# Kernel tuning notes

Hardware: AMD Instinct MI355X
Metric: run time of the kernel (lower is better)

Reference implementation:

```python
import jax, jax.numpy as jnp
import numpy as np

N_NODES = 100000
N_EDGES = 3200000
IN_DIM, HID_DIM, LAT_DIM = 128, 64, 64


def gcn_conv(x, edge_index, W, b):
    """PyG-style GCNConv: add self-loops, symmetric deg^-1/2 normalization,
    linear transform, scatter-add aggregation, bias."""
    N = x.shape[0]
    loops = jnp.arange(N, dtype=edge_index.dtype)
    src = jnp.concatenate([edge_index[0], loops])  # [E+N]
    dst = jnp.concatenate([edge_index[1], loops])  # [E+N]
    # degree on target index (with self loops)
    deg = jax.ops.segment_sum(jnp.ones_like(dst, dtype=x.dtype), dst, num_segments=N)
    dinv = jnp.where(deg > 0, jax.lax.rsqrt(deg), 0.0)
    norm = dinv[src] * dinv[dst]  # [E+N]
    h = x @ W  # [N, out_dim] -- transform BEFORE gather (out_dim <= in_dim)
    msg = h[src] * norm[:, None]  # [E+N, out_dim]
    out = jax.ops.segment_sum(msg, dst, num_segments=N)
    return out + b


def setup_inputs() -> dict:
    key = jax.random.key(0)
    ks = jax.random.split(key, 6)
    x = jax.random.normal(ks[0], (N_NODES, IN_DIM), dtype=jnp.float32)
    edge_index = jax.random.randint(ks[1], (2, N_EDGES), 0, N_NODES, dtype=jnp.int64)
    # Glorot-ish init for weights, zero bias (PyG default)
    W1 = jax.random.normal(ks[2], (IN_DIM, HID_DIM), dtype=jnp.float32) / np.sqrt(IN_DIM)
    b1 = jnp.zeros((HID_DIM,), dtype=jnp.float32)
    W2 = jax.random.normal(ks[3], (HID_DIM, LAT_DIM), dtype=jnp.float32) / np.sqrt(HID_DIM)
    b2 = jnp.zeros((LAT_DIM,), dtype=jnp.float32)
    return {"x": x, "edge_index": edge_index, "W1": W1, "b1": b1, "W2": W2, "b2": b2}


def reference(x, edge_index, W1, b1, W2, b2):
    h = jax.nn.relu(gcn_conv(x, edge_index, W1, b1))
    return gcn_conv(h, edge_index, W2, b2)
```

## Files before the change

### kernel.cpp

```cpp
#include <hip/hip_runtime.h>
#include <cstdint>


#define BSHIFT 7
#define NBMAX 784
#define CH 4096
#define MAXB 6016

typedef __attribute__((ext_vector_type(8))) short bf16x8;
typedef __attribute__((ext_vector_type(4))) float f32x4;

__device__ inline unsigned short f2bf(float f) {
    unsigned u = __float_as_uint(f);
    unsigned r = (u + 0x7FFFu + ((u >> 16) & 1u)) >> 16;
    return (unsigned short)r;
}
__device__ inline unsigned pack2(float a, float b) {
    return (unsigned)f2bf(a) | ((unsigned)f2bf(b) << 16);
}
__device__ inline float blo(unsigned u) { return __uint_as_float(u << 16); }
__device__ inline float bhi(unsigned u) { return __uint_as_float(u & 0xFFFF0000u); }

__global__ __launch_bounds__(256) void hist_kernel(const int* __restrict__ dst,
                                                   int* __restrict__ histmat,
                                                   int E, int nb, int nblk,
                                                   const float* __restrict__ W1,
                                                   const float* __restrict__ W2,
                                                   unsigned short* __restrict__ W1t,
                                                   unsigned short* __restrict__ W2t) {
    if (blockIdx.x >= (unsigned)nblk) {
        int i = (blockIdx.x - nblk) * 256 + threadIdx.x;
        if (i < 128 * 64) {
            int k = i >> 6, n = i & 63;
            W1t[n * 128 + k] = f2bf(W1[i]);
        }
        int j = i - 128 * 64;
        if (j >= 0 && j < 64 * 64) {
            int k = j >> 6, n = j & 63;
            W2t[n * 64 + k] = f2bf(W2[j]);
        }
        return;
    }
    __shared__ int hist[NBMAX];
    int t = threadIdx.x;
    for (int b = t; b < nb; b += 256) hist[b] = 0;
    __syncthreads();
    int base = blockIdx.x * CH;
#pragma unroll
    for (int j = 0; j < CH / 1024; ++j) {
        int idx = base + j * 1024 + t * 4;
        if (idx + 4 <= E) {
            int4 d = *(const int4*)(dst + idx);
            atomicAdd(&hist[d.x >> BSHIFT], 1);
            atomicAdd(&hist[d.y >> BSHIFT], 1);
            atomicAdd(&hist[d.z >> BSHIFT], 1);
            atomicAdd(&hist[d.w >> BSHIFT], 1);
        } else {
            for (int k = 0; k < 4; ++k)
                if (idx + k < E) atomicAdd(&hist[dst[idx + k] >> BSHIFT], 1);
        }
    }
    __syncthreads();
    for (int b = t; b < nb; b += 256) histmat[blockIdx.x * nb + b] = hist[b];
}

__global__ __launch_bounds__(256) void scancol_kernel(const int* __restrict__ histmat,
                                                      int* __restrict__ colbase,
                                                      int* __restrict__ buckettotal,
                                                      int nb, int nblk) {
    __shared__ int ts[256];
    int b = blockIdx.x;
    int t = threadIdx.x;
    int v[4];
    int tsum = 0;
#pragma unroll
    for (int k = 0; k < 4; ++k) {
        int blk = t * 4 + k;
        v[k] = (blk < nblk) ? histmat[blk * nb + b] : 0;
        tsum += v[k];
    }
    ts[t] = tsum;
    __syncthreads();
    for (int ofs = 1; ofs < 256; ofs <<= 1) {
        int val = (t >= ofs) ? ts[t - ofs] : 0;
        __syncthreads();
        ts[t] += val;
        __syncthreads();
    }
    int run = ts[t] - tsum;
#pragma unroll
    for (int k = 0; k < 4; ++k) {
        int blk = t * 4 + k;
        if (blk < nblk) colbase[blk * nb + b] = run;
        run += v[k];
    }
    if (t == 255) buckettotal[b] = ts[255];
}

__global__ __launch_bounds__(256) void scanbucket_kernel(const int* __restrict__ buckettotal,
                                                         int* __restrict__ bucketbase,
                                                         int nb, int E) {
    __shared__ int ts[256];
    int t = threadIdx.x;
    int v[4];
    int tsum = 0;
#pragma unroll
    for (int k = 0; k < 4; ++k) {
        int b = t * 4 + k;
        v[k] = (b < nb) ? buckettotal[b] : 0;
        tsum += v[k];
    }
    ts[t] = tsum;
    __syncthreads();
    for (int ofs = 1; ofs < 256; ofs <<= 1) {
        int val = (t >= ofs) ? ts[t - ofs] : 0;
        __syncthreads();
        ts[t] += val;
        __syncthreads();
    }
    int run = ts[t] - tsum;
#pragma unroll
    for (int k = 0; k < 4; ++k) {
        int b = t * 4 + k;
        if (b < nb) bucketbase[b] = run;
        run += v[k];
    }
    if (t == 0) bucketbase[nb] = E;
}

__global__ __launch_bounds__(256) void bscatter_kernel(const int* __restrict__ src,
                                                       const int* __restrict__ dst,
                                                       const int* __restrict__ colbase,
                                                       const int* __restrict__ bucketbase,
                                                       int* __restrict__ packed,
                                                       int E, int nb) {
    __shared__ int cur[NBMAX];
    int t = threadIdx.x;
    for (int b = t; b < nb; b += 256)
        cur[b] = bucketbase[b] + colbase[blockIdx.x * nb + b];
    __syncthreads();
    int base = blockIdx.x * CH;
#pragma unroll
    for (int j = 0; j < CH / 1024; ++j) {
        int idx = base + j * 1024 + t * 4;
        if (idx + 4 <= E) {
            int4 d = *(const int4*)(dst + idx);
            int4 s = *(const int4*)(src + idx);
            int p;
            p = atomicAdd(&cur[d.x >> BSHIFT], 1); packed[p] = ((d.x & 127) << 17) | s.x;
            p = atomicAdd(&cur[d.y >> BSHIFT], 1); packed[p] = ((d.y & 127) << 17) | s.y;
            p = atomicAdd(&cur[d.z >> BSHIFT], 1); packed[p] = ((d.z & 127) << 17) | s.z;
            p = atomicAdd(&cur[d.w >> BSHIFT], 1); packed[p] = ((d.w & 127) << 17) | s.w;
        } else {
            for (int k = 0; k < 4; ++k)
                if (idx + k < E) {
                    int dd = dst[idx + k], ss = src[idx + k];
                    int p = atomicAdd(&cur[dd >> BSHIFT], 1);
                    packed[p] = ((dd & 127) << 17) | ss;
                }
        }
    }
}

__global__ __launch_bounds__(256) void bcsr_kernel(const int* __restrict__ packed,
                                                   const int* __restrict__ bucketbase,
                                                   int* __restrict__ rowptr,
                                                   float* __restrict__ dinv,
                                                   int* __restrict__ csr,
                                                   int N, int nb) {
    __shared__ int deg[128];
    __shared__ int lrp[128];
    __shared__ int ts[128];
    __shared__ int ebuf[MAXB];
    __shared__ int obuf[MAXB];
    int b = blockIdx.x;
    int t = threadIdx.x;
    if (t < 128) deg[t] = 0;
    __syncthreads();
    int bb0 = bucketbase[b];
    int bb1 = bucketbase[b + 1];
    int cnt = bb1 - bb0;
    bool fits = (cnt <= MAXB);
    if (fits) {
        for (int i = t; i < cnt; i += 256) {
            int v = packed[bb0 + i];
            ebuf[i] = v;
            atomicAdd(&deg[v >> 17], 1);
        }
    } else {
        for (int i = t; i < cnt; i += 256)
            atomicAdd(&deg[packed[bb0 + i] >> 17], 1);
    }
    __syncthreads();
    if (t < 128) ts[t] = deg[t];
    __syncthreads();
    for (int ofs = 1; ofs < 128; ofs <<= 1) {
        int v = (t < 128 && t >= ofs) ? ts[t - ofs] : 0;
        __syncthreads();
        if (t < 128) ts[t] += v;
        __syncthreads();
    }
    int node0 = b << BSHIFT;
    int nlocal = min(128, N - node0);
    if (t < 128) lrp[t] = ts[t] - deg[t];
    if (t < nlocal) {
        rowptr[node0 + t] = bb0 + (ts[t] - deg[t]);
        dinv[node0 + t] = rsqrtf((float)(deg[t] + 1));
    }
    if (t == nlocal) rowptr[node0 + nlocal] = bb1;
    __syncthreads();
    if (fits) {
        for (int i = t; i < cnt; i += 256) {
            int v = ebuf[i];
            int p = atomicAdd(&lrp[v >> 17], 1);
            obuf[p] = v & 0x1FFFF;
        }
        __syncthreads();
        for (int i = t; i < cnt; i += 256) csr[bb0 + i] = obuf[i];
    } else {
        for (int i = t; i < cnt; i += 256) {
            int v = packed[bb0 + i];
            int p = atomicAdd(&lrp[v >> 17], 1);
            csr[bb0 + p] = v & 0x1FFFF;
        }
    }
}

template <int K, bool XBF16>
__global__ __launch_bounds__(256) void gemm_mfma(const void* __restrict__ Xv,
                                                 const unsigned short* __restrict__ Wt,
                                                 const float* __restrict__ dinv,
                                                 unsigned short* __restrict__ Ybf, int M) {
    constexpr int KP = K + 8;
    __shared__ unsigned short Xs[64 * KP];
    __shared__ unsigned short Ws[64 * KP];
    int t = threadIdx.x;
    int row0 = blockIdx.x * 64;

    for (int i = t; i < 64 * K / 8; i += 256) {
        int r = i / (K / 8), c8 = i % (K / 8);
        *(uint4*)(&Ws[r * KP + c8 * 8]) = ((const uint4*)Wt)[i];
    }
    if (XBF16) {
        const unsigned short* X = (const unsigned short*)Xv;
        for (int i = t; i < 64 * K / 8; i += 256) {
            int r = i / (K / 8), c8 = i % (K / 8);
            int gr = row0 + r;
            uint4 v = make_uint4(0u, 0u, 0u, 0u);
            if (gr < M) v = ((const uint4*)(X + (size_t)gr * K))[c8];
            *(uint4*)(&Xs[r * KP + c8 * 8]) = v;
        }
    } else {
        const float* X = (const float*)Xv;
        for (int i = t; i < 64 * K / 4; i += 256) {
            int r = i / (K / 4), c4 = i % (K / 4);
            int gr = row0 + r;
            float4 v = make_float4(0.f, 0.f, 0.f, 0.f);
            if (gr < M) v = ((const float4*)(X + (size_t)gr * K))[c4];
            uint2 p;
            p.x = pack2(v.x, v.y);
            p.y = pack2(v.z, v.w);
            *(uint2*)(&Xs[r * KP + c4 * 4]) = p;
        }
    }
    __syncthreads();

    int lane = t & 63;
    int w = t >> 6;
    int m = lane & 15;
    int q = lane >> 4;

    f32x4 acc[4];
#pragma unroll
    for (int nt = 0; nt < 4; ++nt) acc[nt] = (f32x4){0.f, 0.f, 0.f, 0.f};

#pragma unroll
    for (int s = 0; s < K / 32; ++s) {
        bf16x8 a = *(const bf16x8*)(&Xs[(16 * w + m) * KP + s * 32 + q * 8]);
#pragma unroll
        for (int nt = 0; nt < 4; ++nt) {
            bf16x8 b = *(const bf16x8*)(&Ws[(16 * nt + m) * KP + s * 32 + q * 8]);
            acc[nt] = __builtin_amdgcn_mfma_f32_16x16x32_bf16(a, b, acc[nt], 0, 0, 0);
        }
    }
    __syncthreads();

    unsigned short* Cs = Xs;
#pragma unroll
    for (int nt = 0; nt < 4; ++nt)
#pragma unroll
        for (int r = 0; r < 4; ++r) {
            int row = 16 * w + q * 4 + r;
            int gr = row0 + row;
            float d = (gr < M) ? dinv[gr] : 0.f;
            Cs[row * 72 + nt * 16 + m] = f2bf(acc[nt][r] * d);
        }
    __syncthreads();
    for (int i = t; i < 64 * 64 / 8; i += 256) {
        int r = i >> 3, c8 = i & 7;
        int gr = row0 + r;
        if (gr < M)
            *(uint4*)(Ybf + (size_t)gr * 64 + c8 * 8) = *(const uint4*)(&Cs[r * 72 + c8 * 8]);
    }
}

__global__ __launch_bounds__(256) void aggregate_kernel(const unsigned* __restrict__ hsu,
                                                        const int* __restrict__ rowptr,
                                                        const int* __restrict__ csr,
                                                        const float* __restrict__ dinv,
                                                        const float* __restrict__ bias,
                                                        void* __restrict__ outv, int N,
                                                        int do_relu, int obf) {
    int t = threadIdx.x;
    int node = blockIdx.x * 32 + (t >> 3);
    if (node >= N) return;
    int sub = t & 7;
    int gbase = t & 56;

    float acc[8];
    {
        uint4 v = *(const uint4*)(hsu + (size_t)node * 32 + sub * 4);
        acc[0] = blo(v.x); acc[1] = bhi(v.x);
        acc[2] = blo(v.y); acc[3] = bhi(v.y);
        acc[4] = blo(v.z); acc[5] = bhi(v.z);
        acc[6] = blo(v.w); acc[7] = bhi(v.w);
    }
    int e0 = rowptr[node];
    int e1 = rowptr[node + 1];

    int e = e0;
    for (; e + 8 <= e1; e += 8) {
        int idx = csr[e + sub];
#pragma unroll
        for (int j = 0; j < 8; ++j) {
            int s = __shfl(idx, gbase + j, 64);
            uint4 v = *(const uint4*)(hsu + (size_t)s * 32 + sub * 4);
            acc[0] += blo(v.x); acc[1] += bhi(v.x);
            acc[2] += blo(v.y); acc[3] += bhi(v.y);
            acc[4] += blo(v.z); acc[5] += bhi(v.z);
            acc[6] += blo(v.w); acc[7] += bhi(v.w);
        }
    }
    for (; e < e1; ++e) {
        int s = csr[e];
        uint4 v = *(const uint4*)(hsu + (size_t)s * 32 + sub * 4);
        acc[0] += blo(v.x); acc[1] += bhi(v.x);
        acc[2] += blo(v.y); acc[3] += bhi(v.y);
        acc[4] += blo(v.z); acc[5] += bhi(v.z);
        acc[6] += blo(v.w); acc[7] += bhi(v.w);
    }

    float d = dinv[node];
    float4 b0 = *(const float4*)(bias + sub * 8);
    float4 b1 = *(const float4*)(bias + sub * 8 + 4);
    float o[8];
    o[0] = fmaf(acc[0], d, b0.x); o[1] = fmaf(acc[1], d, b0.y);
    o[2] = fmaf(acc[2], d, b0.z); o[3] = fmaf(acc[3], d, b0.w);
    o[4] = fmaf(acc[4], d, b1.x); o[5] = fmaf(acc[5], d, b1.y);
    o[6] = fmaf(acc[6], d, b1.z); o[7] = fmaf(acc[7], d, b1.w);
    if (do_relu) {
#pragma unroll
        for (int k = 0; k < 8; ++k) o[k] = fmaxf(o[k], 0.f);
    }
    if (obf) {
        unsigned short* outb = (unsigned short*)outv;
        uint4 p;
        p.x = pack2(o[0], o[1]); p.y = pack2(o[2], o[3]);
        p.z = pack2(o[4], o[5]); p.w = pack2(o[6], o[7]);
        *(uint4*)(outb + (size_t)node * 64 + sub * 8) = p;
    } else {
        float* op = (float*)outv + (size_t)node * 64 + sub * 8;
        *(float4*)(op)     = make_float4(o[0], o[1], o[2], o[3]);
        *(float4*)(op + 4) = make_float4(o[4], o[5], o[6], o[7]);
    }
}

extern "C" void kernel_launch(void* const* d_in, const int* in_sizes, int n_in,
                              void* d_out, int out_size, void* d_ws, size_t ws_size,
                              hipStream_t stream) {
    const float* x  = (const float*)d_in[0];
    const int*   ei = (const int*)d_in[1];
    const float* W1 = (const float*)d_in[2];
    const float* b1 = (const float*)d_in[3];
    const float* W2 = (const float*)d_in[4];
    const float* b2 = (const float*)d_in[5];

    const int N = in_sizes[0] / 128;
    const int E = in_sizes[1] / 2;
    const int* src = ei;
    const int* dst = ei + E;
    float* out = (float*)d_out;

    const int nb   = (N + 127) >> BSHIFT;
    const int nblk = (E + CH - 1) / CH;

    char* ws = (char*)d_ws;
    size_t off = 0;
    auto alloc = [&](size_t bytes) -> char* {
        char* p = ws + off;
        off = (off + bytes + 255) & ~(size_t)255;
        return p;
    };
    int*   csr         = (int*)alloc((size_t)E * 4);
    int*   rowptr      = (int*)alloc((size_t)(N + 1) * 4);
    float* dinv        = (float*)alloc((size_t)N * 4);
    int*   bucketbase  = (int*)alloc((size_t)(nb + 1) * 4);
    int*   buckettotal = (int*)alloc((size_t)nb * 4);
    unsigned short* W1t = (unsigned short*)alloc(64 * 128 * 2);
    unsigned short* W2t = (unsigned short*)alloc(64 * 64 * 2);
    unsigned short* bufA = (unsigned short*)alloc((size_t)N * 64 * 2);
    unsigned short* bufB = (unsigned short*)alloc((size_t)N * 64 * 2);
    int* histmat = (int*)bufA;
    int* packed  = (int*)((char*)bufA + ((size_t)nblk * nb * 4 + 255 & ~(size_t)255) + 256);

    hist_kernel<<<nblk + 48, 256, 0, stream>>>(dst, histmat, E, nb, nblk, W1, W2, W1t, W2t);
    scancol_kernel<<<nb, 256, 0, stream>>>(histmat, histmat, buckettotal, nb, nblk);
    scanbucket_kernel<<<1, 256, 0, stream>>>(buckettotal, bucketbase, nb, E);
    bscatter_kernel<<<nblk, 256, 0, stream>>>(src, dst, histmat, bucketbase, packed, E, nb);
    bcsr_kernel<<<nb, 256, 0, stream>>>(packed, bucketbase, rowptr, dinv, csr, N, nb);

    gemm_mfma<128, false><<<(N + 63) / 64, 256, 0, stream>>>(x, W1t, dinv, bufA, N);
    aggregate_kernel<<<(N + 31) / 32, 256, 0, stream>>>((const unsigned*)bufA, rowptr, csr,
                                                        dinv, b1, bufB, N, 1, 1);
    gemm_mfma<64, true><<<(N + 63) / 64, 256, 0, stream>>>(bufB, W2t, dinv, bufA, N);
    aggregate_kernel<<<(N + 31) / 32, 256, 0, stream>>>((const unsigned*)bufA, rowptr, csr,
                                                        dinv, b2, out, N, 0, 0);
}
```

Baseline: 318.8 us.

## Stage bucket scatter through shared memory and unroll gather loop by sixteen

The bucket scatter kernel now builds a local histogram per chunk, prefix-sums it, and groups the chunk's packed edges by bucket in shared memory. It then writes them out contiguously, so global stores become mostly coalesced runs instead of random per-edge stores. The aggregation kernel gains a 16-edge unrolled loop to keep more gather loads in flight. The cost is extra shared memory (about 40KB per block), which may lower occupancy, plus additional syncs and a second pass of LDS atomics.

```diff
diff --git a/kernel.cpp b/kernel.cpp
--- a/kernel.cpp
+++ b/kernel.cpp
@@ -134,32 +134,92 @@
                                                        const int* __restrict__ bucketbase,
                                                        int* __restrict__ packed,
                                                        int E, int nb) {
-    __shared__ int cur[NBMAX];
-    int t = threadIdx.x;
-    for (int b = t; b < nb; b += 256)
-        cur[b] = bucketbase[b] + colbase[blockIdx.x * nb + b];
-    __syncthreads();
+    __shared__ int lofs[NBMAX];
+    __shared__ int lcur[NBMAX];
+    __shared__ int vals[CH];
+    __shared__ int dlt[CH];
+    int t = threadIdx.x;
+    for (int b = t; b < nb; b += 256) lofs[b] = 0;
+    __syncthreads();
+
     int base = blockIdx.x * CH;
+    int n = min(CH, E - base);
+
+    int4 dreg[CH / 1024], sreg[CH / 1024];
 #pragma unroll
     for (int j = 0; j < CH / 1024; ++j) {
         int idx = base + j * 1024 + t * 4;
         if (idx + 4 <= E) {
-            int4 d = *(const int4*)(dst + idx);
-            int4 s = *(const int4*)(src + idx);
-            int p;
-            p = atomicAdd(&cur[d.x >> BSHIFT], 1); packed[p] = ((d.x & 127) << 17) | s.x;
-            p = atomicAdd(&cur[d.y >> BSHIFT], 1); packed[p] = ((d.y & 127) << 17) | s.y;
-            p = atomicAdd(&cur[d.z >> BSHIFT], 1); packed[p] = ((d.z & 127) << 17) | s.z;
-            p = atomicAdd(&cur[d.w >> BSHIFT], 1); packed[p] = ((d.w & 127) << 17) | s.w;
+            dreg[j] = *(const int4*)(dst + idx);
+            sreg[j] = *(const int4*)(src + idx);
+            atomicAdd(&lofs[dreg[j].x >> BSHIFT], 1);
+            atomicAdd(&lofs[dreg[j].y >> BSHIFT], 1);
+            atomicAdd(&lofs[dreg[j].z >> BSHIFT], 1);
+            atomicAdd(&lofs[dreg[j].w >> BSHIFT], 1);
         } else {
-            for (int k = 0; k < 4; ++k)
+            int* dp = (int*)&dreg[j];
+            int* sp = (int*)&sreg[j];
+            for (int k = 0; k < 4; ++k) {
+                dp[k] = -1;
                 if (idx + k < E) {
-                    int dd = dst[idx + k], ss = src[idx + k];
-                    int p = atomicAdd(&cur[dd >> BSHIFT], 1);
-                    packed[p] = ((dd & 127) << 17) | ss;
+                    dp[k] = dst[idx + k];
+                    sp[k] = src[idx + k];
+                    atomicAdd(&lofs[dp[k] >> BSHIFT], 1);
                 }
-        }
-    }
+            }
+        }
+    }
+    __syncthreads();
+
+    {
+        __shared__ int ts[256];
+        int v[4];
+        int tsum = 0;
+#pragma unroll
+        for (int k = 0; k < 4; ++k) {
+            int b = t * 4 + k;
+            v[k] = (b < nb) ? lofs[b] : 0;
+            tsum += v[k];
+        }
+        ts[t] = tsum;
+        __syncthreads();
+        for (int ofs = 1; ofs < 256; ofs <<= 1) {
+            int val = (t >= ofs) ? ts[t - ofs] : 0;
+            __syncthreads();
+            ts[t] += val;
+            __syncthreads();
+        }
+        int run = ts[t] - tsum;
+#pragma unroll
+        for (int k = 0; k < 4; ++k) {
+            int b = t * 4 + k;
+            if (b < nb) {
+                lcur[b] = run;
+                lofs[b] = bucketbase[b] + colbase[blockIdx.x * nb + b] - run;
+            }
+            run += v[k];
+        }
+    }
+    __syncthreads();
+
+#pragma unroll
+    for (int j = 0; j < CH / 1024; ++j) {
+        int* dp = (int*)&dreg[j];
+        int* sp = (int*)&sreg[j];
+#pragma unroll
+        for (int k = 0; k < 4; ++k) {
+            int dd = dp[k];
+            if (dd >= 0) {
+                int b = dd >> BSHIFT;
+                int slot = atomicAdd(&lcur[b], 1);
+                vals[slot] = ((dd & 127) << 17) | sp[k];
+                dlt[slot] = lofs[b];
+            }
+        }
+    }
+    __syncthreads();
+
+    for (int i = t; i < n; i += 256) packed[dlt[i] + i] = vals[i];
 }
 
 __global__ __launch_bounds__(256) void bcsr_kernel(const int* __restrict__ packed,
@@ -329,6 +389,19 @@
     int e1 = rowptr[node + 1];
 
     int e = e0;
+    for (; e + 16 <= e1; e += 16) {
+        int idxA = csr[e + sub];
+        int idxB = csr[e + 8 + sub];
+#pragma unroll
+        for (int j = 0; j < 16; ++j) {
+            int s = __shfl((j < 8) ? idxA : idxB, gbase + (j & 7), 64);
+            uint4 v = *(const uint4*)(hsu + (size_t)s * 32 + sub * 4);
+            acc[0] += blo(v.x); acc[1] += bhi(v.x);
+            acc[2] += blo(v.y); acc[3] += bhi(v.y);
+            acc[4] += blo(v.z); acc[5] += bhi(v.z);
+            acc[6] += blo(v.w); acc[7] += bhi(v.w);
+        }
+    }
     for (; e + 8 <= e1; e += 8) {
         int idx = csr[e + sub];
 #pragma unroll
```

Result: slower. 348.6 us (+9.4%).

## Replace per-block histogram matrix scan with global atomic bucket counts and local staging

Applied to the files above, without the earlier changes.

Replaces the per-block histogram matrix plus column scan with a grid-stride global histogram using atomics and a single bucket scan, folding the weight transpose into the scan kernel. The scatter kernel now computes its own local histogram, reserves global ranges per bucket via atomics, stages edges in shared memory grouped by bucket, then writes them out contiguously. This removes one kernel launch and the histmat read/write traffic, and turns scattered global writes into bucket-grouped runs. In exchange the edge order within each bucket is no longer deterministic, the scatter kernel needs about 70KB of shared memory (reducing occupancy), and the dst array is read twice in the scatter.

```diff
diff --git a/kernel.cpp b/kernel.cpp
--- a/kernel.cpp
+++ b/kernel.cpp
@@ -4,7 +4,7 @@
 
 #define BSHIFT 7
 #define NBMAX 784
-#define CH 4096
+#define CH 8192
 #define MAXB 6016
 
 typedef __attribute__((ext_vector_type(8))) short bf16x8;
@@ -21,34 +21,15 @@
 __device__ inline float blo(unsigned u) { return __uint_as_float(u << 16); }
 __device__ inline float bhi(unsigned u) { return __uint_as_float(u & 0xFFFF0000u); }
 
-__global__ __launch_bounds__(256) void hist_kernel(const int* __restrict__ dst,
-                                                   int* __restrict__ histmat,
-                                                   int E, int nb, int nblk,
-                                                   const float* __restrict__ W1,
-                                                   const float* __restrict__ W2,
-                                                   unsigned short* __restrict__ W1t,
-                                                   unsigned short* __restrict__ W2t) {
-    if (blockIdx.x >= (unsigned)nblk) {
-        int i = (blockIdx.x - nblk) * 256 + threadIdx.x;
-        if (i < 128 * 64) {
-            int k = i >> 6, n = i & 63;
-            W1t[n * 128 + k] = f2bf(W1[i]);
-        }
-        int j = i - 128 * 64;
-        if (j >= 0 && j < 64 * 64) {
-            int k = j >> 6, n = j & 63;
-            W2t[n * 64 + k] = f2bf(W2[j]);
-        }
-        return;
-    }
+__global__ __launch_bounds__(256) void ghist_kernel(const int* __restrict__ dst,
+                                                    int* __restrict__ bucketcount,
+                                                    int E, int nb) {
     __shared__ int hist[NBMAX];
     int t = threadIdx.x;
     for (int b = t; b < nb; b += 256) hist[b] = 0;
     __syncthreads();
-    int base = blockIdx.x * CH;
-#pragma unroll
-    for (int j = 0; j < CH / 1024; ++j) {
-        int idx = base + j * 1024 + t * 4;
+    int stride = gridDim.x * 1024;
+    for (int idx = blockIdx.x * 1024 + t * 4; idx < E; idx += stride) {
         if (idx + 4 <= E) {
             int4 d = *(const int4*)(dst + idx);
             atomicAdd(&hist[d.x >> BSHIFT], 1);
@@ -61,22 +42,41 @@
         }
     }
     __syncthreads();
-    for (int b = t; b < nb; b += 256) histmat[blockIdx.x * nb + b] = hist[b];
-}
-
-__global__ __launch_bounds__(256) void scancol_kernel(const int* __restrict__ histmat,
-                                                      int* __restrict__ colbase,
-                                                      int* __restrict__ buckettotal,
-                                                      int nb, int nblk) {
+    for (int b = t; b < nb; b += 256) {
+        int h = hist[b];
+        if (h) atomicAdd(&bucketcount[b], h);
+    }
+}
+
+__global__ __launch_bounds__(256) void scanbucket_kernel(const int* __restrict__ bucketcount,
+                                                         int* __restrict__ bucketbase,
+                                                         int* __restrict__ buckcur,
+                                                         int nb, int E,
+                                                         const float* __restrict__ W1,
+                                                         const float* __restrict__ W2,
+                                                         unsigned short* __restrict__ W1t,
+                                                         unsigned short* __restrict__ W2t) {
+    if (blockIdx.x > 0) {
+        int i = (blockIdx.x - 1) * 256 + threadIdx.x;
+        if (i < 128 * 64) {
+            int k = i >> 6, n = i & 63;
+            W1t[n * 128 + k] = f2bf(W1[i]);
+        }
+        int j = i - 128 * 64;
+        if (j >= 0 && j < 64 * 64) {
+            int k = j >> 6, n = j & 63;
+            W2t[n * 64 + k] = f2bf(W2[j]);
+        }
+        return;
+    }
     __shared__ int ts[256];
-    int b = blockIdx.x;
     int t = threadIdx.x;
     int v[4];
     int tsum = 0;
 #pragma unroll
     for (int k = 0; k < 4; ++k) {
-        int blk = t * 4 + k;
-        v[k] = (blk < nblk) ? histmat[blk * nb + b] : 0;
+        int b = t * 4 + k;
+        v[k] = (b < nb) ? bucketcount[b] : 0;
         tsum += v[k];
     }
     ts[t] = tsum;
@@ -90,39 +90,11 @@
     int run = ts[t] - tsum;
 #pragma unroll
     for (int k = 0; k < 4; ++k) {
-        int blk = t * 4 + k;
-        if (blk < nblk) colbase[blk * nb + b] = run;
-        run += v[k];
-    }
-    if (t == 255) buckettotal[b] = ts[255];
-}
-
-__global__ __launch_bounds__(256) void scanbucket_kernel(const int* __restrict__ buckettotal,
-                                                         int* __restrict__ bucketbase,
-                                                         int nb, int E) {
-    __shared__ int ts[256];
-    int t = threadIdx.x;
-    int v[4];
-    int tsum = 0;
-#pragma unroll
-    for (int k = 0; k < 4; ++k) {
         int b = t * 4 + k;
-        v[k] = (b < nb) ? buckettotal[b] : 0;
-        tsum += v[k];
-    }
-    ts[t] = tsum;
-    __syncthreads();
-    for (int ofs = 1; ofs < 256; ofs <<= 1) {
-        int val = (t >= ofs) ? ts[t - ofs] : 0;
-        __syncthreads();
-        ts[t] += val;
-        __syncthreads();
-    }
-    int run = ts[t] - tsum;
-#pragma unroll
-    for (int k = 0; k < 4; ++k) {
-        int b = t * 4 + k;
-        if (b < nb) bucketbase[b] = run;
+        if (b < nb) {
+            bucketbase[b] = run;
+            buckcur[b] = run;
+        }
         run += v[k];
     }
     if (t == 0) bucketbase[nb] = E;
@@ -130,36 +102,97 @@
 
 __global__ __launch_bounds__(256) void bscatter_kernel(const int* __restrict__ src,
                                                        const int* __restrict__ dst,
-                                                       const int* __restrict__ colbase,
-                                                       const int* __restrict__ bucketbase,
+                                                       int* __restrict__ buckcur,
                                                        int* __restrict__ packed,
                                                        int E, int nb) {
-    __shared__ int cur[NBMAX];
-    int t = threadIdx.x;
-    for (int b = t; b < nb; b += 256)
-        cur[b] = bucketbase[b] + colbase[blockIdx.x * nb + b];
-    __syncthreads();
+    __shared__ int lofs[NBMAX];
+    __shared__ int lcur[NBMAX];
+    __shared__ int vals[CH];
+    __shared__ int dlt[CH];
+    __shared__ int ts[256];
+    int t = threadIdx.x;
+    for (int b = t; b < nb; b += 256) lofs[b] = 0;
+    __syncthreads();
+
     int base = blockIdx.x * CH;
+    int n = min(CH, E - base);
+
+#pragma unroll
+    for (int j = 0; j < CH / 1024; ++j) {
+        int idx = base + j * 1024 + t * 4;
+        if (idx + 4 <= E) {
+            int4 d = *(const int4*)(dst + idx);
+            atomicAdd(&lofs[d.x >> BSHIFT], 1);
+            atomicAdd(&lofs[d.y >> BSHIFT], 1);
+            atomicAdd(&lofs[d.z >> BSHIFT], 1);
+            atomicAdd(&lofs[d.w >> BSHIFT], 1);
+        } else {
+            for (int k = 0; k < 4; ++k)
+                if (idx + k < E) atomicAdd(&lofs[dst[idx + k] >> BSHIFT], 1);
+        }
+    }
+    __syncthreads();
+
+    {
+        int v[4];
+        int tsum = 0;
+#pragma unroll
+        for (int k = 0; k < 4; ++k) {
+            int b = t * 4 + k;
+            v[k] = (b < nb) ? lofs[b] : 0;
+            tsum += v[k];
+        }
+        ts[t] = tsum;
+        __syncthreads();
+        for (int ofs = 1; ofs < 256; ofs <<= 1) {
+            int val = (t >= ofs) ? ts[t - ofs] : 0;
+            __syncthreads();
+            ts[t] += val;
+            __syncthreads();
+        }
+        int run = ts[t] - tsum;
+#pragma unroll
+        for (int k = 0; k < 4; ++k) {
+            int b = t * 4 + k;
+            if (b < nb) {
+                lcur[b] = run;
+                int g = v[k] ? atomicAdd(&buckcur[b], v[k]) : 0;
+                lofs[b] = g - run;
+            }
+            run += v[k];
+        }
+    }
+    __syncthreads();
+
 #pragma unroll
     for (int j = 0; j < CH / 1024; ++j) {
         int idx = base + j * 1024 + t * 4;
         if (idx + 4 <= E) {
             int4 d = *(const int4*)(dst + idx);
             int4 s = *(const int4*)(src + idx);
-            int p;
-            p = atomicAdd(&cur[d.x >> BSHIFT], 1); packed[p] = ((d.x & 127) << 17) | s.x;
-            p = atomicAdd(&cur[d.y >> BSHIFT], 1); packed[p] = ((d.y & 127) << 17) | s.y;
-            p = atomicAdd(&cur[d.z >> BSHIFT], 1); packed[p] = ((d.z & 127) << 17) | s.z;
-            p = atomicAdd(&cur[d.w >> BSHIFT], 1); packed[p] = ((d.w & 127) << 17) | s.w;
+            int b, slot;
+            b = d.x >> BSHIFT; slot = atomicAdd(&lcur[b], 1);
+            vals[slot] = ((d.x & 127) << 17) | s.x; dlt[slot] = lofs[b];
+            b = d.y >> BSHIFT; slot = atomicAdd(&lcur[b], 1);
+            vals[slot] = ((d.y & 127) << 17) | s.y; dlt[slot] = lofs[b];
+            b = d.z >> BSHIFT; slot = atomicAdd(&lcur[b], 1);
+            vals[slot] = ((d.z & 127) << 17) | s.z; dlt[slot] = lofs[b];
+            b = d.w >> BSHIFT; slot = atomicAdd(&lcur[b], 1);
+            vals[slot] = ((d.w & 127) << 17) | s.w; dlt[slot] = lofs[b];
         } else {
             for (int k = 0; k < 4; ++k)
                 if (idx + k < E) {
                     int dd = dst[idx + k], ss = src[idx + k];
-                    int p = atomicAdd(&cur[dd >> BSHIFT], 1);
-                    packed[p] = ((dd & 127) << 17) | ss;
+                    int b = dd >> BSHIFT;
+                    int slot = atomicAdd(&lcur[b], 1);
+                    vals[slot] = ((dd & 127) << 17) | ss;
+                    dlt[slot] = lofs[b];
                 }
         }
     }
+    __syncthreads();
+
+    for (int i = t; i < n; i += 256) packed[dlt[i] + i] = vals[i];
 }
 
 __global__ __launch_bounds__(256) void bcsr_kernel(const int* __restrict__ packed,
@@ -391,8 +424,8 @@
     const int* dst = ei + E;
     float* out = (float*)d_out;
 
-    const int nb   = (N + 127) >> BSHIFT;
-    const int nblk = (E + CH - 1) / CH;
+    const int nb    = (N + 127) >> BSHIFT;
+    const int nblk  = (E + CH - 1) / CH;
 
     char* ws = (char*)d_ws;
     size_t off = 0;
@@ -405,18 +438,19 @@
     int*   rowptr      = (int*)alloc((size_t)(N + 1) * 4);
     float* dinv        = (float*)alloc((size_t)N * 4);
     int*   bucketbase  = (int*)alloc((size_t)(nb + 1) * 4);
-    int*   buckettotal = (int*)alloc((size_t)nb * 4);
+    int*   bucketcount = (int*)alloc((size_t)nb * 4);
+    int*   buckcur     = (int*)alloc((size_t)nb * 4);
     unsigned short* W1t = (unsigned short*)alloc(64 * 128 * 2);
     unsigned short* W2t = (unsigned short*)alloc(64 * 64 * 2);
     unsigned short* bufA = (unsigned short*)alloc((size_t)N * 64 * 2);
     unsigned short* bufB = (unsigned short*)alloc((size_t)N * 64 * 2);
-    int* histmat = (int*)bufA;
-    int* packed  = (int*)((char*)bufA + ((size_t)nblk * nb * 4 + 255 & ~(size_t)255) + 256);
-
-    hist_kernel<<<nblk + 48, 256, 0, stream>>>(dst, histmat, E, nb, nblk, W1, W2, W1t, W2t);
-    scancol_kernel<<<nb, 256, 0, stream>>>(histmat, histmat, buckettotal, nb, nblk);
-    scanbucket_kernel<<<1, 256, 0, stream>>>(buckettotal, bucketbase, nb, E);
-    bscatter_kernel<<<nblk, 256, 0, stream>>>(src, dst, histmat, bucketbase, packed, E, nb);
+    int* packed = (int*)bufA;
+
+    hipMemsetAsync(bucketcount, 0, (size_t)nb * 4, stream);
+    ghist_kernel<<<256, 256, 0, stream>>>(dst, bucketcount, E, nb);
+    scanbucket_kernel<<<49, 256, 0, stream>>>(bucketcount, bucketbase, buckcur, nb, E,
+                                              W1, W2, W1t, W2t);
+    bscatter_kernel<<<nblk, 256, 0, stream>>>(src, dst, buckcur, packed, E, nb);
     bcsr_kernel<<<nb, 256, 0, stream>>>(packed, bucketbase, rowptr, dinv, csr, N, nb);
 
     gemm_mfma<128, false><<<(N + 63) / 64, 256, 0, stream>>>(x, W1t, dinv, bufA, N);
```

Measured after the change: 323.8 us. Within noise of the previous version (+1.6%).
